# Optimization experiments

Measured on AMD Instinct MI355X. Metric: run time of the kernel, lower is better.

The kernel has to match this reference:

```python
import jax, jax.numpy as jnp
import numpy as np

B, S, D_IN, D_OUT = 4, 2048, 4096, 4096


def setup_inputs() -> dict:
    key = jax.random.key(0)
    k1, k2, k3, k4 = jax.random.split(key, 4)
    x = jax.random.normal(k1, (B, S, D_IN), dtype=jnp.float32)
    # int8-valued weights stored as int32 (values in [-127, 127])
    weight_int8 = jax.random.randint(k2, (D_OUT, D_IN), -127, 128, dtype=jnp.int32)
    # per-output-channel scale, strictly positive (abs-max / 127 style)
    scale = jax.random.uniform(k3, (D_OUT, 1), dtype=jnp.float32, minval=1e-4, maxval=2e-2)
    bias = jax.random.normal(k4, (D_OUT,), dtype=jnp.float32)
    return {"x": x, "weight_int8": weight_int8, "scale": scale, "bias": bias}


def reference(x, weight_int8, scale, bias):
    # Dequantize: per-output-row scale applied to int8 weights -> fp32 [O, I]
    w = weight_int8.astype(jnp.float32) * scale
    # F.linear: y = x @ w^T + b
    out = jnp.einsum('bsi,oi->bso', x, w) + bias
    return out
```

## Files before the change

### kernel.cpp

```cpp
#include <hip/hip_runtime.h>
#include <cstdint>
#include <cstddef>

typedef int i32x4 __attribute__((ext_vector_type(4)));

#define BM 256
#define BN 256
#define BK 64

__device__ __forceinline__ void load16_to_lds(const void* g, void* l) {
  __builtin_amdgcn_global_load_lds(
      (const __attribute__((address_space(1))) void*)g,
      (__attribute__((address_space(3))) void*)l,
      16, 0, 0);
}

__global__ __launch_bounds__(256) void quant_xw(const float* __restrict__ x,
                                                char* __restrict__ xq,
                                                float* __restrict__ sx,
                                                const int* __restrict__ w,
                                                char* __restrict__ wq,
                                                int M, int K) {
  const int t = threadIdx.x;
  __shared__ float red[4];
  if ((int)blockIdx.x < M) {
    const int row = blockIdx.x;
    const float* xr = x + (size_t)row * K;
    float4 v[4];
    float amax = 0.f;
#pragma unroll
    for (int j = 0; j < 4; ++j) {
      v[j] = ((const float4*)xr)[t + j * 256];
      amax = fmaxf(amax, fmaxf(fmaxf(fabsf(v[j].x), fabsf(v[j].y)),
                               fmaxf(fabsf(v[j].z), fabsf(v[j].w))));
    }
#pragma unroll
    for (int off = 32; off; off >>= 1)
      amax = fmaxf(amax, __shfl_xor(amax, off));
    if ((t & 63) == 0) red[t >> 6] = amax;
    __syncthreads();
    amax = fmaxf(fmaxf(red[0], red[1]), fmaxf(red[2], red[3]));
    amax = fmaxf(amax, 1e-20f);

    const float s = 127.0f / amax;
    int* outw = (int*)(xq + (size_t)row * K);
#pragma unroll
    for (int j = 0; j < 4; ++j) {
      int q0 = __float2int_rn(v[j].x * s);
      int q1 = __float2int_rn(v[j].y * s);
      int q2 = __float2int_rn(v[j].z * s);
      int q3 = __float2int_rn(v[j].w * s);
      int pk = (q0 & 0xff) | ((q1 & 0xff) << 8) | ((q2 & 0xff) << 16) | ((q3 & 0xff) << 24);
      outw[t + j * 256] = pk;
    }
    if (t == 0) sx[row] = amax * (1.0f / 127.0f);
  } else {
    const size_t base = (size_t)(blockIdx.x - M) * 4096;
    int* outw = (int*)(wq + base);
#pragma unroll
    for (int j = 0; j < 4; ++j) {
      const int c = t + j * 256;
      int4 a = ((const int4*)(w + base))[c];
      outw[c] = (a.x & 0xff) | ((a.y & 0xff) << 8) | ((a.z & 0xff) << 16) | ((a.w & 0xff) << 24);
    }
  }
}

__global__ __launch_bounds__(512) void gemm_i8_bt(const char* __restrict__ A,
                                                  const char* __restrict__ Bw,
                                                  const float* __restrict__ sx,
                                                  const float* __restrict__ sw,
                                                  const float* __restrict__ bias,
                                                  float* __restrict__ out,
                                                  int M, int N, int K) {
  __shared__ __align__(16) char As[3][BM * BK];
  __shared__ __align__(16) char Bs[3][BN * BK];

  const int tid  = threadIdx.x;
  const int wave = tid >> 6;
  const int lane = tid & 63;
  const int wm   = wave >> 2;
  const int wn   = wave & 3;

  const int gx   = N / BN;
  const int nwg  = gx * (M / BM);
  const int orig = blockIdx.y * gx + blockIdx.x;
  const int wg   = (orig & 7) * (nwg >> 3) + (orig >> 3);
  const int bn   = wg % gx;
  const int bm   = wg / gx;

  i32x4 acc[8][4] = {};

  const int rowT = tid >> 2;
  const int jg   = ((tid & 3) ^ ((tid >> 3) & 3)) << 4;
  const char* Ag1 = A  + (size_t)(bm * BM + rowT) * K + jg;
  const char* Ag2 = Ag1 + (size_t)128 * K;
  const char* Bg1 = Bw + (size_t)(bn * BN + rowT) * K + jg;
  const char* Bg2 = Bg1 + (size_t)128 * K;

  const int ldsO1 = wave << 10;
  const int ldsO2 = 8192 + (wave << 10);

  const int fr  = lane & 15;
  const int swz = (((lane >> 4) ^ ((fr >> 1) & 3)) << 4);
  int offA[8], offB[4];
#pragma unroll
  for (int m = 0; m < 8; ++m) offA[m] = (wm * 128 + m * 16 + fr) * 64 + swz;
#pragma unroll
  for (int n = 0; n < 4; ++n) offB[n] = (wn * 64 + n * 16 + fr) * 64 + swz;

  const int NT = K / BK;

  load16_to_lds(Ag1,      &As[0][ldsO1]);
  load16_to_lds(Ag2,      &As[0][ldsO2]);
  load16_to_lds(Bg1,      &Bs[0][ldsO1]);
  load16_to_lds(Bg2,      &Bs[0][ldsO2]);
  load16_to_lds(Ag1 + BK, &As[1][ldsO1]);
  load16_to_lds(Ag2 + BK, &As[1][ldsO2]);
  load16_to_lds(Bg1 + BK, &Bs[1][ldsO1]);
  load16_to_lds(Bg2 + BK, &Bs[1][ldsO2]);
  asm volatile("s_waitcnt vmcnt(4)" ::: "memory");
  __builtin_amdgcn_s_barrier();
  __builtin_amdgcn_sched_barrier(0);

  int buf = 0;
  for (int t = 0; t < NT; ++t) {
    const int  nb = (buf >= 1) ? buf - 1 : 2;
    const size_t ko = (size_t)(t + 2) * BK;
    const bool pf = (t + 2) < NT;

    if (pf) {
      load16_to_lds(Ag1 + ko, &As[nb][ldsO1]);
      load16_to_lds(Ag2 + ko, &As[nb][ldsO2]);
      load16_to_lds(Bg1 + ko, &Bs[nb][ldsO1]);
      load16_to_lds(Bg2 + ko, &Bs[nb][ldsO2]);
    }

    i32x4 a0 = *(const i32x4*)&As[buf][offA[0]];
    i32x4 a1 = *(const i32x4*)&As[buf][offA[1]];
    i32x4 a2 = *(const i32x4*)&As[buf][offA[2]];
    i32x4 a3 = *(const i32x4*)&As[buf][offA[3]];
    i32x4 b0 = *(const i32x4*)&Bs[buf][offB[0]];
    i32x4 b1 = *(const i32x4*)&Bs[buf][offB[1]];
    i32x4 b2 = *(const i32x4*)&Bs[buf][offB[2]];
    i32x4 b3 = *(const i32x4*)&Bs[buf][offB[3]];
    i32x4 a4 = *(const i32x4*)&As[buf][offA[4]];
    i32x4 a5 = *(const i32x4*)&As[buf][offA[5]];
    i32x4 a6 = *(const i32x4*)&As[buf][offA[6]];
    i32x4 a7 = *(const i32x4*)&As[buf][offA[7]];

    __builtin_amdgcn_s_setprio(1);
    acc[0][0] = __builtin_amdgcn_mfma_i32_16x16x64_i8(a0, b0, acc[0][0], 0, 0, 0);
    acc[0][1] = __builtin_amdgcn_mfma_i32_16x16x64_i8(a0, b1, acc[0][1], 0, 0, 0);
    acc[0][2] = __builtin_amdgcn_mfma_i32_16x16x64_i8(a0, b2, acc[0][2], 0, 0, 0);
    acc[0][3] = __builtin_amdgcn_mfma_i32_16x16x64_i8(a0, b3, acc[0][3], 0, 0, 0);
    acc[1][0] = __builtin_amdgcn_mfma_i32_16x16x64_i8(a1, b0, acc[1][0], 0, 0, 0);
    acc[1][1] = __builtin_amdgcn_mfma_i32_16x16x64_i8(a1, b1, acc[1][1], 0, 0, 0);
    acc[1][2] = __builtin_amdgcn_mfma_i32_16x16x64_i8(a1, b2, acc[1][2], 0, 0, 0);
    acc[1][3] = __builtin_amdgcn_mfma_i32_16x16x64_i8(a1, b3, acc[1][3], 0, 0, 0);
    acc[2][0] = __builtin_amdgcn_mfma_i32_16x16x64_i8(a2, b0, acc[2][0], 0, 0, 0);
    acc[2][1] = __builtin_amdgcn_mfma_i32_16x16x64_i8(a2, b1, acc[2][1], 0, 0, 0);
    acc[2][2] = __builtin_amdgcn_mfma_i32_16x16x64_i8(a2, b2, acc[2][2], 0, 0, 0);
    acc[2][3] = __builtin_amdgcn_mfma_i32_16x16x64_i8(a2, b3, acc[2][3], 0, 0, 0);
    acc[3][0] = __builtin_amdgcn_mfma_i32_16x16x64_i8(a3, b0, acc[3][0], 0, 0, 0);
    acc[3][1] = __builtin_amdgcn_mfma_i32_16x16x64_i8(a3, b1, acc[3][1], 0, 0, 0);
    acc[3][2] = __builtin_amdgcn_mfma_i32_16x16x64_i8(a3, b2, acc[3][2], 0, 0, 0);
    acc[3][3] = __builtin_amdgcn_mfma_i32_16x16x64_i8(a3, b3, acc[3][3], 0, 0, 0);
    acc[4][0] = __builtin_amdgcn_mfma_i32_16x16x64_i8(a4, b0, acc[4][0], 0, 0, 0);
    acc[4][1] = __builtin_amdgcn_mfma_i32_16x16x64_i8(a4, b1, acc[4][1], 0, 0, 0);
    acc[4][2] = __builtin_amdgcn_mfma_i32_16x16x64_i8(a4, b2, acc[4][2], 0, 0, 0);
    acc[4][3] = __builtin_amdgcn_mfma_i32_16x16x64_i8(a4, b3, acc[4][3], 0, 0, 0);
    acc[5][0] = __builtin_amdgcn_mfma_i32_16x16x64_i8(a5, b0, acc[5][0], 0, 0, 0);
    acc[5][1] = __builtin_amdgcn_mfma_i32_16x16x64_i8(a5, b1, acc[5][1], 0, 0, 0);
    acc[5][2] = __builtin_amdgcn_mfma_i32_16x16x64_i8(a5, b2, acc[5][2], 0, 0, 0);
    acc[5][3] = __builtin_amdgcn_mfma_i32_16x16x64_i8(a5, b3, acc[5][3], 0, 0, 0);
    acc[6][0] = __builtin_amdgcn_mfma_i32_16x16x64_i8(a6, b0, acc[6][0], 0, 0, 0);
    acc[6][1] = __builtin_amdgcn_mfma_i32_16x16x64_i8(a6, b1, acc[6][1], 0, 0, 0);
    acc[6][2] = __builtin_amdgcn_mfma_i32_16x16x64_i8(a6, b2, acc[6][2], 0, 0, 0);
    acc[6][3] = __builtin_amdgcn_mfma_i32_16x16x64_i8(a6, b3, acc[6][3], 0, 0, 0);
    acc[7][0] = __builtin_amdgcn_mfma_i32_16x16x64_i8(a7, b0, acc[7][0], 0, 0, 0);
    acc[7][1] = __builtin_amdgcn_mfma_i32_16x16x64_i8(a7, b1, acc[7][1], 0, 0, 0);
    acc[7][2] = __builtin_amdgcn_mfma_i32_16x16x64_i8(a7, b2, acc[7][2], 0, 0, 0);
    acc[7][3] = __builtin_amdgcn_mfma_i32_16x16x64_i8(a7, b3, acc[7][3], 0, 0, 0);
    __builtin_amdgcn_s_setprio(0);

    if (pf)                 { asm volatile("s_waitcnt vmcnt(4)" ::: "memory"); }
    else if (t + 1 < NT)    { asm volatile("s_waitcnt vmcnt(0)" ::: "memory"); }
    __builtin_amdgcn_s_barrier();
    __builtin_amdgcn_sched_barrier(0);

    buf = (buf < 2) ? buf + 1 : 0;
  }

  const int colc = lane & 15;
  const int rq   = (lane >> 4) << 2;
  float sxv[8][4];
#pragma unroll
  for (int m = 0; m < 8; ++m) {
    const int row0 = bm * BM + wm * 128 + m * 16 + rq;
#pragma unroll
    for (int r = 0; r < 4; ++r) sxv[m][r] = sx[row0 + r];
  }
#pragma unroll
  for (int n = 0; n < 4; ++n) {
    const int col = bn * BN + wn * 64 + n * 16 + colc;
    const float sc = sw[col];
    const float bi = bias[col];
#pragma unroll
    for (int m = 0; m < 8; ++m) {
      const int row0 = bm * BM + wm * 128 + m * 16 + rq;
#pragma unroll
      for (int r = 0; r < 4; ++r)
        out[(size_t)(row0 + r) * N + col] = (float)acc[m][n][r] * (sxv[m][r] * sc) + bi;
    }
  }
}

extern "C" void kernel_launch(void* const* d_in, const int* in_sizes, int n_in,
                              void* d_out, int out_size, void* d_ws, size_t ws_size,
                              hipStream_t stream) {
  const float* x     = (const float*)d_in[0];
  const int*   w     = (const int*)d_in[1];
  const float* scale = (const float*)d_in[2];
  const float* bias  = (const float*)d_in[3];
  float*       out   = (float*)d_out;

  const int N = in_sizes[3];
  const int K = in_sizes[1] / N;
  const int M = in_sizes[0] / K;

  char*  xq = (char*)d_ws;
  char*  wq = xq + (size_t)M * K;
  float* sx = (float*)(wq + (size_t)N * K);

  const unsigned wblocks = (unsigned)(((size_t)N * K) / 4096);
  quant_xw<<<dim3((unsigned)M + wblocks), dim3(256), 0, stream>>>(x, xq, sx, w, wq, M, K);

  gemm_i8_bt<<<dim3(N / BN, M / BM), dim3(512), 0, stream>>>(xq, wq, sx, scale, bias, out, M, N, K);
}
```

Baseline: 447.2 us.

## Use 16 waves per GEMM tile with split-phase load/MFMA interleaving

Doubles the workgroup to 1024 threads (16 waves) over the same 256x256 tile, so each wave now owns a 64x64 sub-tile with half the accumulators. The inner loop is split into two phases with extra barriers: the A-tile prefetch is issued alongside the first half of the MFMAs and the B-tile prefetch alongside the second half. The goal is more waves to hide latency and lower register pressure per wave. The cost is more barriers per K step, and each A/B fragment loaded from LDS feeds fewer MFMAs, so LDS read traffic per MFMA goes up.

```diff
diff --git a/kernel.cpp b/kernel.cpp
--- a/kernel.cpp
+++ b/kernel.cpp
@@ -66,13 +66,13 @@
   }
 }
 
-__global__ __launch_bounds__(512) void gemm_i8_bt(const char* __restrict__ A,
-                                                  const char* __restrict__ Bw,
-                                                  const float* __restrict__ sx,
-                                                  const float* __restrict__ sw,
-                                                  const float* __restrict__ bias,
-                                                  float* __restrict__ out,
-                                                  int M, int N, int K) {
+__global__ __launch_bounds__(1024) void gemm_i8_bt(const char* __restrict__ A,
+                                                   const char* __restrict__ Bw,
+                                                   const float* __restrict__ sx,
+                                                   const float* __restrict__ sw,
+                                                   const float* __restrict__ bias,
+                                                   float* __restrict__ out,
+                                                   int M, int N, int K) {
   __shared__ __align__(16) char As[3][BM * BK];
   __shared__ __align__(16) char Bs[3][BN * BK];
 
@@ -89,66 +89,49 @@
   const int bn   = wg % gx;
   const int bm   = wg / gx;
 
-  i32x4 acc[8][4] = {};
+  i32x4 acc[4][4] = {};
 
   const int rowT = tid >> 2;
   const int jg   = ((tid & 3) ^ ((tid >> 3) & 3)) << 4;
-  const char* Ag1 = A  + (size_t)(bm * BM + rowT) * K + jg;
-  const char* Ag2 = Ag1 + (size_t)128 * K;
-  const char* Bg1 = Bw + (size_t)(bn * BN + rowT) * K + jg;
-  const char* Bg2 = Bg1 + (size_t)128 * K;
-
-  const int ldsO1 = wave << 10;
-  const int ldsO2 = 8192 + (wave << 10);
+  const char* Ag = A  + (size_t)(bm * BM + rowT) * K + jg;
+  const char* Bg = Bw + (size_t)(bn * BN + rowT) * K + jg;
+
+  const int ldsO = wave << 10;
 
   const int fr  = lane & 15;
   const int swz = (((lane >> 4) ^ ((fr >> 1) & 3)) << 4);
-  int offA[8], offB[4];
-#pragma unroll
-  for (int m = 0; m < 8; ++m) offA[m] = (wm * 128 + m * 16 + fr) * 64 + swz;
+  int offA[4], offB[4];
+#pragma unroll
+  for (int m = 0; m < 4; ++m) offA[m] = (wm * 64 + m * 16 + fr) * 64 + swz;
 #pragma unroll
   for (int n = 0; n < 4; ++n) offB[n] = (wn * 64 + n * 16 + fr) * 64 + swz;
 
   const int NT = K / BK;
 
-  load16_to_lds(Ag1,      &As[0][ldsO1]);
-  load16_to_lds(Ag2,      &As[0][ldsO2]);
-  load16_to_lds(Bg1,      &Bs[0][ldsO1]);
-  load16_to_lds(Bg2,      &Bs[0][ldsO2]);
-  load16_to_lds(Ag1 + BK, &As[1][ldsO1]);
-  load16_to_lds(Ag2 + BK, &As[1][ldsO2]);
-  load16_to_lds(Bg1 + BK, &Bs[1][ldsO1]);
-  load16_to_lds(Bg2 + BK, &Bs[1][ldsO2]);
-  asm volatile("s_waitcnt vmcnt(4)" ::: "memory");
+  load16_to_lds(Ag,      &As[0][ldsO]);
+  load16_to_lds(Bg,      &Bs[0][ldsO]);
+  load16_to_lds(Ag + BK, &As[1][ldsO]);
+  load16_to_lds(Bg + BK, &Bs[1][ldsO]);
+  asm volatile("s_waitcnt vmcnt(2)" ::: "memory");
   __builtin_amdgcn_s_barrier();
-  __builtin_amdgcn_sched_barrier(0);
 
   int buf = 0;
   for (int t = 0; t < NT; ++t) {
     const int  nb = (buf >= 1) ? buf - 1 : 2;
     const size_t ko = (size_t)(t + 2) * BK;
     const bool pf = (t + 2) < NT;
-
-    if (pf) {
-      load16_to_lds(Ag1 + ko, &As[nb][ldsO1]);
-      load16_to_lds(Ag2 + ko, &As[nb][ldsO2]);
-      load16_to_lds(Bg1 + ko, &Bs[nb][ldsO1]);
-      load16_to_lds(Bg2 + ko, &Bs[nb][ldsO2]);
-    }
+    const bool rd = (t + 1) < NT;
 
     i32x4 a0 = *(const i32x4*)&As[buf][offA[0]];
     i32x4 a1 = *(const i32x4*)&As[buf][offA[1]];
-    i32x4 a2 = *(const i32x4*)&As[buf][offA[2]];
-    i32x4 a3 = *(const i32x4*)&As[buf][offA[3]];
     i32x4 b0 = *(const i32x4*)&Bs[buf][offB[0]];
     i32x4 b1 = *(const i32x4*)&Bs[buf][offB[1]];
     i32x4 b2 = *(const i32x4*)&Bs[buf][offB[2]];
     i32x4 b3 = *(const i32x4*)&Bs[buf][offB[3]];
-    i32x4 a4 = *(const i32x4*)&As[buf][offA[4]];
-    i32x4 a5 = *(const i32x4*)&As[buf][offA[5]];
-    i32x4 a6 = *(const i32x4*)&As[buf][offA[6]];
-    i32x4 a7 = *(const i32x4*)&As[buf][offA[7]];
-
+    if (pf) load16_to_lds(Ag + ko, &As[nb][ldsO]);
+    __builtin_amdgcn_s_barrier();
+    asm volatile("s_waitcnt lgkmcnt(0)" ::: "memory");
+    __builtin_amdgcn_sched_barrier(0);
     __builtin_amdgcn_s_setprio(1);
     acc[0][0] = __builtin_amdgcn_mfma_i32_16x16x64_i8(a0, b0, acc[0][0], 0, 0, 0);
     acc[0][1] = __builtin_amdgcn_mfma_i32_16x16x64_i8(a0, b1, acc[0][1], 0, 0, 0);
@@ -158,6 +141,16 @@
     acc[1][1] = __builtin_amdgcn_mfma_i32_16x16x64_i8(a1, b1, acc[1][1], 0, 0, 0);
     acc[1][2] = __builtin_amdgcn_mfma_i32_16x16x64_i8(a1, b2, acc[1][2], 0, 0, 0);
     acc[1][3] = __builtin_amdgcn_mfma_i32_16x16x64_i8(a1, b3, acc[1][3], 0, 0, 0);
+    __builtin_amdgcn_s_setprio(0);
+    __builtin_amdgcn_s_barrier();
+
+    i32x4 a2 = *(const i32x4*)&As[buf][offA[2]];
+    i32x4 a3 = *(const i32x4*)&As[buf][offA[3]];
+    if (pf) load16_to_lds(Bg + ko, &Bs[nb][ldsO]);
+    __builtin_amdgcn_s_barrier();
+    asm volatile("s_waitcnt lgkmcnt(0)" ::: "memory");
+    __builtin_amdgcn_sched_barrier(0);
+    __builtin_amdgcn_s_setprio(1);
     acc[2][0] = __builtin_amdgcn_mfma_i32_16x16x64_i8(a2, b0, acc[2][0], 0, 0, 0);
     acc[2][1] = __builtin_amdgcn_mfma_i32_16x16x64_i8(a2, b1, acc[2][1], 0, 0, 0);
     acc[2][2] = __builtin_amdgcn_mfma_i32_16x16x64_i8(a2, b2, acc[2][2], 0, 0, 0);
@@ -166,38 +159,21 @@
     acc[3][1] = __builtin_amdgcn_mfma_i32_16x16x64_i8(a3, b1, acc[3][1], 0, 0, 0);
     acc[3][2] = __builtin_amdgcn_mfma_i32_16x16x64_i8(a3, b2, acc[3][2], 0, 0, 0);
     acc[3][3] = __builtin_amdgcn_mfma_i32_16x16x64_i8(a3, b3, acc[3][3], 0, 0, 0);
-    acc[4][0] = __builtin_amdgcn_mfma_i32_16x16x64_i8(a4, b0, acc[4][0], 0, 0, 0);
-    acc[4][1] = __builtin_amdgcn_mfma_i32_16x16x64_i8(a4, b1, acc[4][1], 0, 0, 0);
-    acc[4][2] = __builtin_amdgcn_mfma_i32_16x16x64_i8(a4, b2, acc[4][2], 0, 0, 0);
-    acc[4][3] = __builtin_amdgcn_mfma_i32_16x16x64_i8(a4, b3, acc[4][3], 0, 0, 0);
-    acc[5][0] = __builtin_amdgcn_mfma_i32_16x16x64_i8(a5, b0, acc[5][0], 0, 0, 0);
-    acc[5][1] = __builtin_amdgcn_mfma_i32_16x16x64_i8(a5, b1, acc[5][1], 0, 0, 0);
-    acc[5][2] = __builtin_amdgcn_mfma_i32_16x16x64_i8(a5, b2, acc[5][2], 0, 0, 0);
-    acc[5][3] = __builtin_amdgcn_mfma_i32_16x16x64_i8(a5, b3, acc[5][3], 0, 0, 0);
-    acc[6][0] = __builtin_amdgcn_mfma_i32_16x16x64_i8(a6, b0, acc[6][0], 0, 0, 0);
-    acc[6][1] = __builtin_amdgcn_mfma_i32_16x16x64_i8(a6, b1, acc[6][1], 0, 0, 0);
-    acc[6][2] = __builtin_amdgcn_mfma_i32_16x16x64_i8(a6, b2, acc[6][2], 0, 0, 0);
-    acc[6][3] = __builtin_amdgcn_mfma_i32_16x16x64_i8(a6, b3, acc[6][3], 0, 0, 0);
-    acc[7][0] = __builtin_amdgcn_mfma_i32_16x16x64_i8(a7, b0, acc[7][0], 0, 0, 0);
-    acc[7][1] = __builtin_amdgcn_mfma_i32_16x16x64_i8(a7, b1, acc[7][1], 0, 0, 0);
-    acc[7][2] = __builtin_amdgcn_mfma_i32_16x16x64_i8(a7, b2, acc[7][2], 0, 0, 0);
-    acc[7][3] = __builtin_amdgcn_mfma_i32_16x16x64_i8(a7, b3, acc[7][3], 0, 0, 0);
     __builtin_amdgcn_s_setprio(0);
 
-    if (pf)                 { asm volatile("s_waitcnt vmcnt(4)" ::: "memory"); }
-    else if (t + 1 < NT)    { asm volatile("s_waitcnt vmcnt(0)" ::: "memory"); }
-    __builtin_amdgcn_s_barrier();
-    __builtin_amdgcn_sched_barrier(0);
+    if (pf)          { asm volatile("s_waitcnt vmcnt(2)" ::: "memory"); }
+    else if (rd)     { asm volatile("s_waitcnt vmcnt(0)" ::: "memory"); }
+    __builtin_amdgcn_s_barrier();
 
     buf = (buf < 2) ? buf + 1 : 0;
   }
 
   const int colc = lane & 15;
   const int rq   = (lane >> 4) << 2;
-  float sxv[8][4];
-#pragma unroll
-  for (int m = 0; m < 8; ++m) {
-    const int row0 = bm * BM + wm * 128 + m * 16 + rq;
+  float sxv[4][4];
+#pragma unroll
+  for (int m = 0; m < 4; ++m) {
+    const int row0 = bm * BM + wm * 64 + m * 16 + rq;
 #pragma unroll
     for (int r = 0; r < 4; ++r) sxv[m][r] = sx[row0 + r];
   }
@@ -207,8 +183,8 @@
     const float sc = sw[col];
     const float bi = bias[col];
 #pragma unroll
-    for (int m = 0; m < 8; ++m) {
-      const int row0 = bm * BM + wm * 128 + m * 16 + rq;
+    for (int m = 0; m < 4; ++m) {
+      const int row0 = bm * BM + wm * 64 + m * 16 + rq;
 #pragma unroll
       for (int r = 0; r < 4; ++r)
         out[(size_t)(row0 + r) * N + col] = (float)acc[m][n][r] * (sxv[m][r] * sc) + bi;
@@ -236,5 +212,5 @@
   const unsigned wblocks = (unsigned)(((size_t)N * K) / 4096);
   quant_xw<<<dim3((unsigned)M + wblocks), dim3(256), 0, stream>>>(x, xq, sx, w, wq, M, K);
 
-  gemm_i8_bt<<<dim3(N / BN, M / BM), dim3(512), 0, stream>>>(xq, wq, sx, scale, bias, out, M, N, K);
-}
+  gemm_i8_bt<<<dim3(N / BN, M / BM), dim3(1024), 0, stream>>>(xq, wq, sx, scale, bias, out, M, N, K);
+}
```

New measurement: 416.6 us. 1.07x faster.
